# Optimization experiments

Measured on AMD Instinct MI355X. Metric: run time of the kernel, lower is better.

The kernel has to match this reference:

```python
import jax, jax.numpy as jnp
import numpy as np

K = 9
KS = (K - 1) // 2  # k_self
C_LIGHT = 299792458.0 / 1e6 / 600.0  # speed of light in detector units (as in HLayer)
BN_EPS = 1e-3  # keras BatchNormalization default epsilon


def _win2(f):
    # (B, N) -> (B, N, K): out[b, n, k] = f[b, n + k - KS], zero-padded at boundaries
    B, N = f.shape
    fp = jnp.pad(f, ((0, 0), (KS, KS)))
    return jnp.stack([fp[:, k:k + N] for k in range(K)], axis=2)


def _win3(f):
    # (B, N, F) -> (B, N, K, F): same shift-window along N
    B, N, F = f.shape
    fp = jnp.pad(f, ((0, 0), (KS, KS), (0, 0)))
    return jnp.stack([fp[:, k:k + N, :] for k in range(K)], axis=2)


def _valid_mask(N):
    # (N, K): True where neighbor index n + k - KS is in range
    idx = jnp.arange(N)[:, None] + jnp.arange(K)[None, :] - KS
    return (idx >= 0) & (idx < N)


def _hlayer(x):
    # x: (B, N, 6) with cols (t, c, a, px, py, pz) -> (B, N, K, 12)
    t, c, a = x[..., 0], x[..., 1], x[..., 2]
    px, py, pz = x[..., 3], x[..., 4], x[..., 5]
    N = x.shape[1]
    valid = _valid_mask(N)[None, :, :]  # (1, N, K)

    def d(f):  # shifted minus self, zeroed at boundaries (matches TF pad of the diff)
        return jnp.where(valid, _win2(f) - f[:, :, None], 0.0)

    dt, dx, dy, dz = d(t), d(px), d(py), d(pz)
    eu2 = dx * dx + dy * dy + dz * dz
    euclidean = jnp.sqrt(eu2)
    lorentz = (C_LIGHT * dt) ** 2 - eu2
    feats = [_win2(t), _win2(px), _win2(py), _win2(pz), _win2(c), _win2(a),
             dt, dx, dy, dz, euclidean, lorentz]
    return jnp.stack(feats, axis=3)  # (B, N, K, 12)


def _conv_bn(x, W, b, gamma, beta, mean, var):
    # kernel-size-1 Conv1D with relu activation, then inference-mode BatchNorm
    y = jax.nn.relu(jnp.matmul(x, W) + b)
    return gamma * (y - mean) * jax.lax.rsqrt(var + BN_EPS) + beta


def _make_params(key, dims):
    params = {}
    for i, (fi, fo) in enumerate(zip(dims[:-1], dims[1:])):
        key, k1 = jax.random.split(key)
        s = np.sqrt(2.0 / fi)
        params[f'W{i}'] = jax.random.normal(k1, (fi, fo), jnp.float32) * s
        params[f'b{i}'] = jnp.zeros((fo,), jnp.float32)
        key, k2, k3, k4 = jax.random.split(key, 4)
        params[f'g{i}'] = 1.0 + 0.1 * jax.random.normal(k2, (fo,), jnp.float32)
        params[f'be{i}'] = 0.1 * jax.random.normal(k3, (fo,), jnp.float32)
        params[f'mu{i}'] = 0.1 * jax.random.normal(k4, (fo,), jnp.float32)
        params[f'var{i}'] = 0.5 + jax.random.uniform(key, (fo,), jnp.float32)
    return params


def setup_inputs() -> dict:
    key = jax.random.key(0)
    kx, km, kf = jax.random.split(key, 3)
    B, N = 8, 4096
    x = jax.random.normal(kx, (B, N, 6), jnp.float32)
    dims_m = [12, 128, 256]   # MLayer/CRLayer stack on H features
    dims_f = [6, 128, 256]    # FRLayer stack on raw inputs
    pm = _make_params(km, dims_m)
    pf = _make_params(kf, dims_f)
    inp = {'x': x}
    for i in range(2):
        for n in ['W', 'b', 'g', 'be', 'mu', 'var']:
            inp[f'm_{n}{i}'] = pm[f'{n}{i}']
            inp[f'f_{n}{i}'] = pf[f'{n}{i}']
    return inp


def reference(x,
              m_W0, m_b0, m_g0, m_be0, m_mu0, m_var0,
              m_W1, m_b1, m_g1, m_be1, m_mu1, m_var1,
              f_W0, f_b0, f_g0, f_be0, f_mu0, f_var0,
              f_W1, f_b1, f_g1, f_be1, f_mu1, f_var1):
    # H-layer: (B, N, 6) -> (B, N, K, 12) geometric neighbor features
    h = _hlayer(x)
    # M branch (CRLayer, 1x1 convs over feature dim): -> m_nkf (B, N, K, 256)
    m = _conv_bn(h, m_W0, m_b0, m_g0, m_be0, m_mu0, m_var0)
    m = _conv_bn(m, m_W1, m_b1, m_g1, m_be1, m_mu1, m_var1)
    # FR branch on raw inputs: -> fr_nf (B, N, 256)
    fr = _conv_bn(x, f_W0, f_b0, f_g0, f_be0, f_mu0, f_var0)
    fr = _conv_bn(fr, f_W1, f_b1, f_g1, f_be1, f_mu1, f_var1)
    # A-layer: gate shifted fr by m and max-aggregate over K neighbors
    fr_sh = _win3(fr)                      # (B, N, K, 256), zero-padded shifts
    T = m * fr_sh                          # (B, N, K, 256)
    return jnp.max(T, axis=2)              # (B, N, 256)
```

## Files before the change

kernel.cpp:

```cpp
#include <hip/hip_runtime.h>
#include <hip/hip_bf16.h>

#define N_PTS 4096
#define C_LIGHT 0.49965409666666664f
#define BN_EPS 1e-3f

typedef __attribute__((ext_vector_type(8))) short short8;
typedef __attribute__((ext_vector_type(4))) float f32x4;

static __device__ __forceinline__ unsigned short f2bf(float f) {
    unsigned u = __float_as_uint(f);
    u += 0x7FFFu + ((u >> 16) & 1u);
    return (unsigned short)(u >> 16);
}
static __device__ __forceinline__ float bf2f(unsigned short h) {
    return __uint_as_float(((unsigned)h) << 16);
}
static __device__ __forceinline__ unsigned pk2(float a, float b) {
    __hip_bfloat162 h = __float22bfloat162_rn(make_float2(a, b));
    union { __hip_bfloat162 v; unsigned u; } cv;
    cv.v = h;
    return cv.u;
}

__global__ __launch_bounds__(256) void fold_kernel(
    const float* __restrict__ mW1, const float* __restrict__ mb1,
    const float* __restrict__ mg0, const float* __restrict__ mbe0,
    const float* __restrict__ mmu0, const float* __restrict__ mvar0,
    const float* __restrict__ mg1, const float* __restrict__ mbe1,
    const float* __restrict__ mmu1, const float* __restrict__ mvar1,
    const float* __restrict__ fW1p, const float* __restrict__ fb1,
    const float* __restrict__ fg0, const float* __restrict__ fbe0,
    const float* __restrict__ fmu0, const float* __restrict__ fvar0,
    const float* __restrict__ fg1, const float* __restrict__ fbe1,
    const float* __restrict__ fmu1, const float* __restrict__ fvar1,
    float* __restrict__ mBf, float* __restrict__ mS1, float* __restrict__ mT1,
    unsigned short* __restrict__ mWhi, unsigned short* __restrict__ mWlo,
    float* __restrict__ fBf, float* __restrict__ fS1, float* __restrict__ fT1,
    unsigned short* __restrict__ fWhi, unsigned short* __restrict__ fWlo)
{
    int br = blockIdx.x;
    const float* W1  = br ? fW1p : mW1;
    const float* b1  = br ? fb1  : mb1;
    const float* g0  = br ? fg0  : mg0;
    const float* be0 = br ? fbe0 : mbe0;
    const float* mu0 = br ? fmu0 : mmu0;
    const float* var0= br ? fvar0: mvar0;
    const float* g1  = br ? fg1  : mg1;
    const float* be1 = br ? fbe1 : mbe1;
    const float* mu1 = br ? fmu1 : mmu1;
    const float* var1= br ? fvar1: mvar1;
    float* Bf = br ? fBf : mBf;
    float* S1 = br ? fS1 : mS1;
    float* T1 = br ? fT1 : mT1;
    unsigned short* Whi = br ? fWhi : mWhi;
    unsigned short* Wlo = br ? fWlo : mWlo;

    __shared__ float s0s[128], t0s[128];
    int t = threadIdx.x;
    if (t < 128) {
        float s = g0[t] / sqrtf(var0[t] + BN_EPS);
        s0s[t] = s;
        t0s[t] = be0[t] - mu0[t] * s;
    }
    __syncthreads();

    {
        float s1 = g1[t] / sqrtf(var1[t] + BN_EPS);
        S1[t] = s1;
        T1[t] = be1[t] - mu1[t] * s1;
        float acc = b1[t];
        for (int i = 0; i < 128; ++i) acc = fmaf(t0s[i], W1[i * 256 + t], acc);
        Bf[t] = acc;
    }

    for (int e = t; e < 32768; e += 256) {
        int j = e & 7, l = (e >> 3) & 63, ks = (e >> 9) & 3, ct = e >> 11;
        int i = ks * 32 + (l >> 4) * 8 + j;
        int c = ct * 16 + (l & 15);
        float w = s0s[i] * W1[i * 256 + c];
        unsigned short hi = f2bf(w);
        unsigned short lo = f2bf(w - bf2f(hi));
        Whi[e] = hi;
        Wlo[e] = lo;
    }
}

__global__ __launch_bounds__(256, 2) void fr_kernel(
    const float* __restrict__ x,
    const float* __restrict__ W0,
    const float* __restrict__ b0,
    const short8* __restrict__ WfHi, const short8* __restrict__ WfLo,
    const float* __restrict__ Bf, const float* __restrict__ S1,
    const float* __restrict__ T1,
    float* __restrict__ frT)
{
    __shared__ float xs[64][6];
    __shared__ __attribute__((aligned(16))) float w0s[6][136];
    __shared__ __attribute__((aligned(16))) float b0s[128];
    __shared__ __attribute__((aligned(16))) unsigned short hAhi[4 * 64 * 8];
    __shared__ __attribute__((aligned(16))) unsigned short hAlo[4 * 64 * 8];

    int t = threadIdx.x;
    long row0 = (long)blockIdx.x * 64;

    for (int i = t; i < 384; i += 256) xs[i / 6][i % 6] = x[row0 * 6 + i];
    for (int i = t; i < 768; i += 256) w0s[i >> 7][i & 127] = W0[i];
    if (t < 128) b0s[t] = b0[t];

    int lane = t & 63, wv = t >> 6;
    int laneN = lane & 15, laneH = lane >> 4;
    int cg = t & 7;

    float bfv[4], s1v[4], t1v[4];
    int colc[4];
#pragma unroll
    for (int c = 0; c < 4; ++c) {
        colc[c] = (wv * 4 + c) * 16 + laneN;
        bfv[c] = Bf[colc[c]];
        s1v[c] = S1[colc[c]];
        t1v[c] = T1[colc[c]];
    }
    f32x4 acc[4][4];
#pragma unroll
    for (int mt = 0; mt < 4; ++mt)
#pragma unroll
        for (int c = 0; c < 4; ++c) {
            f32x4 z = {bfv[c], bfv[c], bfv[c], bfv[c]};
            acc[mt][c] = z;
        }
    __syncthreads();

    for (int ks = 0; ks < 4; ++ks) {
        int k0 = ks * 32 + cg * 4;
        float4 wreg[6];
#pragma unroll
        for (int i = 0; i < 6; ++i) wreg[i] = *(const float4*)&w0s[i][k0];
        float4 bq = *(const float4*)&b0s[k0];

        for (int idx = t; idx < 512; idx += 256) {
            int row = idx >> 3;
            float a0 = bq.x, a1 = bq.y, a2 = bq.z, a3 = bq.w;
#pragma unroll
            for (int i = 0; i < 6; ++i) {
                float hv = xs[row][i];
                a0 = fmaf(hv, wreg[i].x, a0);
                a1 = fmaf(hv, wreg[i].y, a1);
                a2 = fmaf(hv, wreg[i].z, a2);
                a3 = fmaf(hv, wreg[i].w, a3);
            }
            a0 = fmaxf(a0, 0.f); a1 = fmaxf(a1, 0.f);
            a2 = fmaxf(a2, 0.f); a3 = fmaxf(a3, 0.f);
            unsigned hi01 = pk2(a0, a1), hi23 = pk2(a2, a3);
            float q0 = __uint_as_float(hi01 << 16);
            float q1 = __uint_as_float(hi01 & 0xffff0000u);
            float q2 = __uint_as_float(hi23 << 16);
            float q3 = __uint_as_float(hi23 & 0xffff0000u);
            unsigned lo01 = pk2(a0 - q0, a1 - q1), lo23 = pk2(a2 - q2, a3 - q3);
            int mt = row >> 4, nl = row & 15;
            int base = (mt * 64 + (cg >> 1) * 16 + nl) * 8 + (cg & 1) * 4;
            *(uint2*)&hAhi[base] = make_uint2(hi01, hi23);
            *(uint2*)&hAlo[base] = make_uint2(lo01, lo23);
        }
        __syncthreads();

        short8 Bhi[4], Blo[4];
#pragma unroll
        for (int c = 0; c < 4; ++c) {
            int fo = ((wv * 4 + c) * 4 + ks) * 64 + lane;
            Bhi[c] = WfHi[fo];
            Blo[c] = WfLo[fo];
        }
#pragma unroll
        for (int mt = 0; mt < 4; ++mt) {
            short8 Ahi = *(const short8*)&hAhi[(mt * 64 + lane) * 8];
            short8 Alo = *(const short8*)&hAlo[(mt * 64 + lane) * 8];
#pragma unroll
            for (int c = 0; c < 4; ++c) {
                f32x4 a = acc[mt][c];
                a = __builtin_amdgcn_mfma_f32_16x16x32_bf16(Alo, Bhi[c], a, 0, 0, 0);
                a = __builtin_amdgcn_mfma_f32_16x16x32_bf16(Ahi, Blo[c], a, 0, 0, 0);
                a = __builtin_amdgcn_mfma_f32_16x16x32_bf16(Ahi, Bhi[c], a, 0, 0, 0);
                acc[mt][c] = a;
            }
        }
        __syncthreads();
    }

#pragma unroll
    for (int c = 0; c < 4; ++c)
#pragma unroll
        for (int mt = 0; mt < 4; ++mt) {
            float4 o;
            o.x = fmaf(fmaxf(acc[mt][c][0], 0.f), s1v[c], t1v[c]);
            o.y = fmaf(fmaxf(acc[mt][c][1], 0.f), s1v[c], t1v[c]);
            o.z = fmaf(fmaxf(acc[mt][c][2], 0.f), s1v[c], t1v[c]);
            o.w = fmaf(fmaxf(acc[mt][c][3], 0.f), s1v[c], t1v[c]);
            *(float4*)&frT[(long)colc[c] * 32768 + row0 + mt * 16 + laneH * 4] = o;
        }
}

#define SM_XS   0
#define SM_B0   576
#define SM_W0   1088
#define SM_HF   7616
#define SM_AHI  14528
#define SM_ALO  23744
#define SM_FRT  0
#define SM_OUT  33792
#define SM_TOT  50432

__global__ __launch_bounds__(256, 2) void fused_kernel(
    const float* __restrict__ x,
    const float* __restrict__ W0,
    const float* __restrict__ b0,
    const short8* __restrict__ WfHi, const short8* __restrict__ WfLo,
    const float* __restrict__ Bf, const float* __restrict__ S1,
    const float* __restrict__ T1,
    const float* __restrict__ frT,
    float* __restrict__ out)
{
    __shared__ __attribute__((aligned(16))) char smem[SM_TOT];
    float* xs  = (float*)(smem + SM_XS);
    float* b0s = (float*)(smem + SM_B0);
    float* w0s = (float*)(smem + SM_W0);
    float* hfp = (float*)(smem + SM_HF);
    unsigned short* hAhi = (unsigned short*)(smem + SM_AHI);
    unsigned short* hAlo = (unsigned short*)(smem + SM_ALO);
    float* frL = (float*)(smem + SM_FRT);
    float* oL  = (float*)(smem + SM_OUT);

    int t = threadIdx.x;
    int bn = blockIdx.x;
    int b  = bn >> 8;
    int n0 = (bn & 255) << 4;
    const float* xb = x + (long)b * N_PTS * 6;

    if (t < 144) {
        int rr = t / 6, cc = t % 6;
        int n = n0 - 4 + rr;
        xs[rr * 6 + cc] = (n >= 0 && n < N_PTS) ? xb[n * 6 + cc] : 0.f;
    }
    for (int i = t; i < 12 * 128; i += 256) w0s[(i >> 7) * 136 + (i & 127)] = W0[i];
    if (t < 128) b0s[t] = b0[t];
    __syncthreads();

    if (t < 144) {
        int kt = t >> 4, nl = t & 15;
        const float* self = &xs[(nl + 4) * 6];
        const float* nb   = &xs[(nl + kt) * 6];
        int nbn = n0 + nl + kt - 4;
        float msk = (nbn >= 0 && nbn < N_PTS) ? 1.f : 0.f;
        float dt = (nb[0] - self[0]) * msk;
        float dx = (nb[3] - self[3]) * msk;
        float dy = (nb[4] - self[4]) * msk;
        float dz = (nb[5] - self[5]) * msk;
        float eu2 = dx * dx + dy * dy + dz * dz;
        float* h = &hfp[t * 12];
        h[0]  = nb[0];
        h[1]  = nb[3];
        h[2]  = nb[4];
        h[3]  = nb[5];
        h[4]  = nb[1];
        h[5]  = nb[2];
        h[6]  = dt;
        h[7]  = dx;
        h[8]  = dy;
        h[9]  = dz;
        h[10] = sqrtf(eu2);
        float cdt = C_LIGHT * dt;
        h[11] = cdt * cdt - eu2;
    }

    int lane = t & 63, wv = t >> 6;
    int laneN = lane & 15, laneH = lane >> 4;
    int cg = t & 7;

    float bfv[4], s1v[4], t1v[4];
    int colc[4];
#pragma unroll
    for (int c = 0; c < 4; ++c) {
        colc[c] = (wv * 4 + c) * 16 + laneN;
        bfv[c] = Bf[colc[c]];
        s1v[c] = S1[colc[c]];
        t1v[c] = T1[colc[c]];
    }
    f32x4 acc[9][4];
#pragma unroll
    for (int kt = 0; kt < 9; ++kt)
#pragma unroll
        for (int c = 0; c < 4; ++c) {
            f32x4 z = {bfv[c], bfv[c], bfv[c], bfv[c]};
            acc[kt][c] = z;
        }
    __syncthreads();

    for (int ks = 0; ks < 4; ++ks) {
        int k0 = ks * 32 + cg * 4;
        float4 wreg[12];
#pragma unroll
        for (int i = 0; i < 12; ++i) wreg[i] = *(const float4*)&w0s[i * 136 + k0];
        float4 bq = *(const float4*)&b0s[k0];

        for (int idx = t; idx < 1152; idx += 256) {
            int row = idx >> 3;
            float a0 = bq.x, a1 = bq.y, a2 = bq.z, a3 = bq.w;
#pragma unroll
            for (int i = 0; i < 12; ++i) {
                float hv = hfp[row * 12 + i];
                a0 = fmaf(hv, wreg[i].x, a0);
                a1 = fmaf(hv, wreg[i].y, a1);
                a2 = fmaf(hv, wreg[i].z, a2);
                a3 = fmaf(hv, wreg[i].w, a3);
            }
            a0 = fmaxf(a0, 0.f); a1 = fmaxf(a1, 0.f);
            a2 = fmaxf(a2, 0.f); a3 = fmaxf(a3, 0.f);
            unsigned hi01 = pk2(a0, a1), hi23 = pk2(a2, a3);
            float q0 = __uint_as_float(hi01 << 16);
            float q1 = __uint_as_float(hi01 & 0xffff0000u);
            float q2 = __uint_as_float(hi23 << 16);
            float q3 = __uint_as_float(hi23 & 0xffff0000u);
            unsigned lo01 = pk2(a0 - q0, a1 - q1), lo23 = pk2(a2 - q2, a3 - q3);
            int kt = row >> 4, nl = row & 15;
            int base = (kt * 64 + (cg >> 1) * 16 + nl) * 8 + (cg & 1) * 4;
            *(uint2*)&hAhi[base] = make_uint2(hi01, hi23);
            *(uint2*)&hAlo[base] = make_uint2(lo01, lo23);
        }
        __syncthreads();

        short8 Bhi[4], Blo[4];
#pragma unroll
        for (int c = 0; c < 4; ++c) {
            int fo = ((wv * 4 + c) * 4 + ks) * 64 + lane;
            Bhi[c] = WfHi[fo];
            Blo[c] = WfLo[fo];
        }
#pragma unroll
        for (int kt = 0; kt < 9; ++kt) {
            short8 Ahi = *(const short8*)&hAhi[(kt * 64 + lane) * 8];
            short8 Alo = *(const short8*)&hAlo[(kt * 64 + lane) * 8];
#pragma unroll
            for (int c = 0; c < 4; ++c) {
                f32x4 a = acc[kt][c];
                a = __builtin_amdgcn_mfma_f32_16x16x32_bf16(Alo, Bhi[c], a, 0, 0, 0);
                a = __builtin_amdgcn_mfma_f32_16x16x32_bf16(Ahi, Blo[c], a, 0, 0, 0);
                a = __builtin_amdgcn_mfma_f32_16x16x32_bf16(Ahi, Bhi[c], a, 0, 0, 0);
                acc[kt][c] = a;
            }
        }
        __syncthreads();
    }
    for (int i = t; i < 2048; i += 256) {
        int col = i >> 3, seg = i & 7;
        int nn = n0 - 8 + seg * 4;
        float4 v = make_float4(0.f, 0.f, 0.f, 0.f);
        if (nn >= 0 && nn < N_PTS)
            v = *(const float4*)&frT[(long)col * 32768 + (b << 12) + nn];
        *(float4*)&frL[col * 33 + seg * 4] = v;
    }
    __syncthreads();

#pragma unroll
    for (int c = 0; c < 4; ++c) {
        float fv[12];
        int fb = colc[c] * 33 + laneH * 4 + 4;
#pragma unroll
        for (int j = 0; j < 12; ++j) fv[j] = frL[fb + j];
#pragma unroll
        for (int r = 0; r < 4; ++r) {
            float best;
#pragma unroll
            for (int kt = 0; kt < 9; ++kt) {
                float m = fmaf(fmaxf(acc[kt][c][r], 0.f), s1v[c], t1v[c]);
                float T = m * fv[r + kt];
                best = (kt == 0) ? T : fmaxf(best, T);
            }
            oL[(laneH * 4 + r) * 260 + colc[c]] = best;
        }
    }
    __syncthreads();

    float* outb = out + ((long)b << 20);
    for (int i = t; i < 1024; i += 256) {
        int row = i >> 6, c4 = (i & 63) << 2;
        float4 v = *(const float4*)&oL[row * 260 + c4];
        *(float4*)&outb[((long)(n0 + row) << 8) + c4] = v;
    }
}

extern "C" void kernel_launch(void* const* d_in, const int* in_sizes, int n_in,
                              void* d_out, int out_size, void* d_ws, size_t ws_size,
                              hipStream_t stream)
{
    const float* x = (const float*)d_in[0];
    const float* m_W0  = (const float*)d_in[1];
    const float* f_W0  = (const float*)d_in[2];
    const float* m_b0  = (const float*)d_in[3];
    const float* f_b0  = (const float*)d_in[4];
    const float* m_g0  = (const float*)d_in[5];
    const float* f_g0  = (const float*)d_in[6];
    const float* m_be0 = (const float*)d_in[7];
    const float* f_be0 = (const float*)d_in[8];
    const float* m_mu0 = (const float*)d_in[9];
    const float* f_mu0 = (const float*)d_in[10];
    const float* m_var0= (const float*)d_in[11];
    const float* f_var0= (const float*)d_in[12];
    const float* m_W1  = (const float*)d_in[13];
    const float* f_W1  = (const float*)d_in[14];
    const float* m_b1  = (const float*)d_in[15];
    const float* f_b1  = (const float*)d_in[16];
    const float* m_g1  = (const float*)d_in[17];
    const float* f_g1  = (const float*)d_in[18];
    const float* m_be1 = (const float*)d_in[19];
    const float* f_be1 = (const float*)d_in[20];
    const float* m_mu1 = (const float*)d_in[21];
    const float* f_mu1 = (const float*)d_in[22];
    const float* m_var1= (const float*)d_in[23];
    const float* f_var1= (const float*)d_in[24];

    char* wsb = (char*)d_ws;
    float* frT = (float*)wsb;
    float* mBf = (float*)(wsb + 33554432);
    float* mS1 = mBf + 256;
    float* mT1 = mS1 + 256;
    float* fBf = mT1 + 256;
    float* fS1 = fBf + 256;
    float* fT1 = fS1 + 256;
    unsigned short* mWhi = (unsigned short*)(fT1 + 256);
    unsigned short* mWlo = mWhi + 32768;
    unsigned short* fWhi = mWlo + 32768;
    unsigned short* fWlo = fWhi + 32768;

    fold_kernel<<<2, 256, 0, stream>>>(
        m_W1, m_b1, m_g0, m_be0, m_mu0, m_var0, m_g1, m_be1, m_mu1, m_var1,
        f_W1, f_b1, f_g0, f_be0, f_mu0, f_var0, f_g1, f_be1, f_mu1, f_var1,
        mBf, mS1, mT1, mWhi, mWlo,
        fBf, fS1, fT1, fWhi, fWlo);

    fr_kernel<<<8 * N_PTS / 64, 256, 0, stream>>>(
        x, f_W0, f_b0, (const short8*)fWhi, (const short8*)fWlo,
        fBf, fS1, fT1, frT);

    fused_kernel<<<8 * N_PTS / 16, 256, 0, stream>>>(
        x, m_W0, m_b0, (const short8*)mWhi, (const short8*)mWlo,
        mBf, mS1, mT1, frT, (float*)d_out);
}
```

Baseline: 239.6 us.

## Fuse FR branch into main kernel with halo recompute and parallelize weight folding

```diff
diff --git a/kernel.cpp b/kernel.cpp
--- a/kernel.cpp
+++ b/kernel.cpp
@@ -23,7 +23,7 @@
     return cv.u;
 }
 
-__global__ __launch_bounds__(256) void fold_kernel(
+__global__ __launch_bounds__(256) void fold_all(
     const float* __restrict__ mW1, const float* __restrict__ mb1,
     const float* __restrict__ mg0, const float* __restrict__ mbe0,
     const float* __restrict__ mmu0, const float* __restrict__ mvar0,
@@ -35,200 +35,106 @@
     const float* __restrict__ fg1, const float* __restrict__ fbe1,
     const float* __restrict__ fmu1, const float* __restrict__ fvar1,
     float* __restrict__ mBf, float* __restrict__ mS1, float* __restrict__ mT1,
+    float* __restrict__ fBf, float* __restrict__ fS1, float* __restrict__ fT1,
     unsigned short* __restrict__ mWhi, unsigned short* __restrict__ mWlo,
-    float* __restrict__ fBf, float* __restrict__ fS1, float* __restrict__ fT1,
     unsigned short* __restrict__ fWhi, unsigned short* __restrict__ fWlo)
 {
-    int br = blockIdx.x;
-    const float* W1  = br ? fW1p : mW1;
-    const float* b1  = br ? fb1  : mb1;
-    const float* g0  = br ? fg0  : mg0;
-    const float* be0 = br ? fbe0 : mbe0;
-    const float* mu0 = br ? fmu0 : mmu0;
-    const float* var0= br ? fvar0: mvar0;
-    const float* g1  = br ? fg1  : mg1;
-    const float* be1 = br ? fbe1 : mbe1;
-    const float* mu1 = br ? fmu1 : mmu1;
-    const float* var1= br ? fvar1: mvar1;
-    float* Bf = br ? fBf : mBf;
-    float* S1 = br ? fS1 : mS1;
-    float* T1 = br ? fT1 : mT1;
-    unsigned short* Whi = br ? fWhi : mWhi;
-    unsigned short* Wlo = br ? fWlo : mWlo;
-
-    __shared__ float s0s[128], t0s[128];
+    int bid = blockIdx.x;
     int t = threadIdx.x;
-    if (t < 128) {
-        float s = g0[t] / sqrtf(var0[t] + BN_EPS);
-        s0s[t] = s;
-        t0s[t] = be0[t] - mu0[t] * s;
-    }
-    __syncthreads();
-
-    {
+
+    if (bid < 2) {
+        int br = bid;
+        const float* W1  = br ? fW1p : mW1;
+        const float* b1  = br ? fb1  : mb1;
+        const float* g0  = br ? fg0  : mg0;
+        const float* be0 = br ? fbe0 : mbe0;
+        const float* mu0 = br ? fmu0 : mmu0;
+        const float* var0= br ? fvar0: mvar0;
+        const float* g1  = br ? fg1  : mg1;
+        const float* be1 = br ? fbe1 : mbe1;
+        const float* mu1 = br ? fmu1 : mmu1;
+        const float* var1= br ? fvar1: mvar1;
+        float* Bf = br ? fBf : mBf;
+        float* S1 = br ? fS1 : mS1;
+        float* T1 = br ? fT1 : mT1;
+
+        __shared__ float t0s[128];
+        if (t < 128) {
+            float s = g0[t] / sqrtf(var0[t] + BN_EPS);
+            t0s[t] = be0[t] - mu0[t] * s;
+        }
+        __syncthreads();
+
         float s1 = g1[t] / sqrtf(var1[t] + BN_EPS);
         S1[t] = s1;
         T1[t] = be1[t] - mu1[t] * s1;
         float acc = b1[t];
         for (int i = 0; i < 128; ++i) acc = fmaf(t0s[i], W1[i * 256 + t], acc);
         Bf[t] = acc;
-    }
-
-    for (int e = t; e < 32768; e += 256) {
-        int j = e & 7, l = (e >> 3) & 63, ks = (e >> 9) & 3, ct = e >> 11;
-        int i = ks * 32 + (l >> 4) * 8 + j;
+    } else {
+        int wbid = bid - 2;
+        int br = wbid >> 4, blk = wbid & 15;
+        const float* W1  = br ? fW1p : mW1;
+        const float* g0  = br ? fg0  : mg0;
+        const float* var0= br ? fvar0: mvar0;
+        unsigned short* Whi = br ? fWhi : mWhi;
+        unsigned short* Wlo = br ? fWlo : mWlo;
+
+        __shared__ float s0s[128];
+        if (t < 128) s0s[t] = g0[t] / sqrtf(var0[t] + BN_EPS);
+        __syncthreads();
+
+        int e0 = blk * 2048 + t * 8;
+        int l = (e0 >> 3) & 63, ks = (e0 >> 9) & 3, ct = e0 >> 11;
         int c = ct * 16 + (l & 15);
-        float w = s0s[i] * W1[i * 256 + c];
-        unsigned short hi = f2bf(w);
-        unsigned short lo = f2bf(w - bf2f(hi));
-        Whi[e] = hi;
-        Wlo[e] = lo;
-    }
-}
-
-__global__ __launch_bounds__(256, 2) void fr_kernel(
-    const float* __restrict__ x,
-    const float* __restrict__ W0,
-    const float* __restrict__ b0,
-    const short8* __restrict__ WfHi, const short8* __restrict__ WfLo,
-    const float* __restrict__ Bf, const float* __restrict__ S1,
-    const float* __restrict__ T1,
-    float* __restrict__ frT)
-{
-    __shared__ float xs[64][6];
-    __shared__ __attribute__((aligned(16))) float w0s[6][136];
-    __shared__ __attribute__((aligned(16))) float b0s[128];
-    __shared__ __attribute__((aligned(16))) unsigned short hAhi[4 * 64 * 8];
-    __shared__ __attribute__((aligned(16))) unsigned short hAlo[4 * 64 * 8];
-
-    int t = threadIdx.x;
-    long row0 = (long)blockIdx.x * 64;
-
-    for (int i = t; i < 384; i += 256) xs[i / 6][i % 6] = x[row0 * 6 + i];
-    for (int i = t; i < 768; i += 256) w0s[i >> 7][i & 127] = W0[i];
-    if (t < 128) b0s[t] = b0[t];
-
-    int lane = t & 63, wv = t >> 6;
-    int laneN = lane & 15, laneH = lane >> 4;
-    int cg = t & 7;
-
-    float bfv[4], s1v[4], t1v[4];
-    int colc[4];
-#pragma unroll
-    for (int c = 0; c < 4; ++c) {
-        colc[c] = (wv * 4 + c) * 16 + laneN;
-        bfv[c] = Bf[colc[c]];
-        s1v[c] = S1[colc[c]];
-        t1v[c] = T1[colc[c]];
-    }
-    f32x4 acc[4][4];
-#pragma unroll
-    for (int mt = 0; mt < 4; ++mt)
-#pragma unroll
-        for (int c = 0; c < 4; ++c) {
-            f32x4 z = {bfv[c], bfv[c], bfv[c], bfv[c]};
-            acc[mt][c] = z;
-        }
-    __syncthreads();
-
-    for (int ks = 0; ks < 4; ++ks) {
-        int k0 = ks * 32 + cg * 4;
-        float4 wreg[6];
-#pragma unroll
-        for (int i = 0; i < 6; ++i) wreg[i] = *(const float4*)&w0s[i][k0];
-        float4 bq = *(const float4*)&b0s[k0];
-
-        for (int idx = t; idx < 512; idx += 256) {
-            int row = idx >> 3;
-            float a0 = bq.x, a1 = bq.y, a2 = bq.z, a3 = bq.w;
-#pragma unroll
-            for (int i = 0; i < 6; ++i) {
-                float hv = xs[row][i];
-                a0 = fmaf(hv, wreg[i].x, a0);
-                a1 = fmaf(hv, wreg[i].y, a1);
-                a2 = fmaf(hv, wreg[i].z, a2);
-                a3 = fmaf(hv, wreg[i].w, a3);
-            }
-            a0 = fmaxf(a0, 0.f); a1 = fmaxf(a1, 0.f);
-            a2 = fmaxf(a2, 0.f); a3 = fmaxf(a3, 0.f);
-            unsigned hi01 = pk2(a0, a1), hi23 = pk2(a2, a3);
-            float q0 = __uint_as_float(hi01 << 16);
-            float q1 = __uint_as_float(hi01 & 0xffff0000u);
-            float q2 = __uint_as_float(hi23 << 16);
-            float q3 = __uint_as_float(hi23 & 0xffff0000u);
-            unsigned lo01 = pk2(a0 - q0, a1 - q1), lo23 = pk2(a2 - q2, a3 - q3);
-            int mt = row >> 4, nl = row & 15;
-            int base = (mt * 64 + (cg >> 1) * 16 + nl) * 8 + (cg & 1) * 4;
-            *(uint2*)&hAhi[base] = make_uint2(hi01, hi23);
-            *(uint2*)&hAlo[base] = make_uint2(lo01, lo23);
-        }
-        __syncthreads();
-
-        short8 Bhi[4], Blo[4];
-#pragma unroll
-        for (int c = 0; c < 4; ++c) {
-            int fo = ((wv * 4 + c) * 4 + ks) * 64 + lane;
-            Bhi[c] = WfHi[fo];
-            Blo[c] = WfLo[fo];
-        }
-#pragma unroll
-        for (int mt = 0; mt < 4; ++mt) {
-            short8 Ahi = *(const short8*)&hAhi[(mt * 64 + lane) * 8];
-            short8 Alo = *(const short8*)&hAlo[(mt * 64 + lane) * 8];
-#pragma unroll
-            for (int c = 0; c < 4; ++c) {
-                f32x4 a = acc[mt][c];
-                a = __builtin_amdgcn_mfma_f32_16x16x32_bf16(Alo, Bhi[c], a, 0, 0, 0);
-                a = __builtin_amdgcn_mfma_f32_16x16x32_bf16(Ahi, Blo[c], a, 0, 0, 0);
-                a = __builtin_amdgcn_mfma_f32_16x16x32_bf16(Ahi, Bhi[c], a, 0, 0, 0);
-                acc[mt][c] = a;
-            }
-        }
-        __syncthreads();
-    }
-
-#pragma unroll
-    for (int c = 0; c < 4; ++c)
-#pragma unroll
-        for (int mt = 0; mt < 4; ++mt) {
-            float4 o;
-            o.x = fmaf(fmaxf(acc[mt][c][0], 0.f), s1v[c], t1v[c]);
-            o.y = fmaf(fmaxf(acc[mt][c][1], 0.f), s1v[c], t1v[c]);
-            o.z = fmaf(fmaxf(acc[mt][c][2], 0.f), s1v[c], t1v[c]);
-            o.w = fmaf(fmaxf(acc[mt][c][3], 0.f), s1v[c], t1v[c]);
-            *(float4*)&frT[(long)colc[c] * 32768 + row0 + mt * 16 + laneH * 4] = o;
-        }
-}
-
-#define SM_XS   0
-#define SM_B0   576
-#define SM_W0   1088
-#define SM_HF   7616
-#define SM_AHI  14528
-#define SM_ALO  23744
-#define SM_FRT  0
-#define SM_OUT  33792
-#define SM_TOT  50432
+        int ib = ks * 32 + (l >> 4) * 8;
+        unsigned short hi[8], lo[8];
+#pragma unroll
+        for (int j = 0; j < 8; ++j) {
+            float w = s0s[ib + j] * W1[(ib + j) * 256 + c];
+            hi[j] = f2bf(w);
+            lo[j] = f2bf(w - bf2f(hi[j]));
+        }
+        *(uint4*)&Whi[e0] = *(uint4*)hi;
+        *(uint4*)&Wlo[e0] = *(uint4*)lo;
+    }
+}
+
+#define SM_XS    0
+#define SM_B0F   768
+#define SM_W0F   1280
+#define SM_B0M   4544
+#define SM_W0M   5056
+#define SM_HF    11584
+#define SM_FRFRG 18496
+#define SM_MFRG  22592
+#define SM_OUT   22592
+#define SM_FRL   41024
+#define SM_TOT   74304
 
 __global__ __launch_bounds__(256, 2) void fused_kernel(
     const float* __restrict__ x,
-    const float* __restrict__ W0,
-    const float* __restrict__ b0,
-    const short8* __restrict__ WfHi, const short8* __restrict__ WfLo,
-    const float* __restrict__ Bf, const float* __restrict__ S1,
-    const float* __restrict__ T1,
-    const float* __restrict__ frT,
+    const float* __restrict__ mW0,
+    const float* __restrict__ mb0,
+    const float* __restrict__ fW0,
+    const float* __restrict__ fb0,
+    const short8* __restrict__ mWfHi, const short8* __restrict__ mWfLo,
+    const short8* __restrict__ fWfHi, const short8* __restrict__ fWfLo,
+    const float* __restrict__ mBf, const float* __restrict__ mS1,
+    const float* __restrict__ mT1,
+    const float* __restrict__ fBf, const float* __restrict__ fS1,
+    const float* __restrict__ fT1,
     float* __restrict__ out)
 {
     __shared__ __attribute__((aligned(16))) char smem[SM_TOT];
-    float* xs  = (float*)(smem + SM_XS);
-    float* b0s = (float*)(smem + SM_B0);
-    float* w0s = (float*)(smem + SM_W0);
-    float* hfp = (float*)(smem + SM_HF);
-    unsigned short* hAhi = (unsigned short*)(smem + SM_AHI);
-    unsigned short* hAlo = (unsigned short*)(smem + SM_ALO);
-    float* frL = (float*)(smem + SM_FRT);
-    float* oL  = (float*)(smem + SM_OUT);
+    float* xs   = (float*)(smem + SM_XS);
+    float* b0f  = (float*)(smem + SM_B0F);
+    float* w0f  = (float*)(smem + SM_W0F);
+    float* b0m  = (float*)(smem + SM_B0M);
+    float* w0m  = (float*)(smem + SM_W0M);
+    float* hfp  = (float*)(smem + SM_HF);
+    float* frL  = (float*)(smem + SM_FRL);
+    float* oL   = (float*)(smem + SM_OUT);
 
     int t = threadIdx.x;
     int bn = blockIdx.x;
@@ -236,19 +142,20 @@
     int n0 = (bn & 255) << 4;
     const float* xb = x + (long)b * N_PTS * 6;
 
-    if (t < 144) {
+    if (t < 192) {
         int rr = t / 6, cc = t % 6;
-        int n = n0 - 4 + rr;
+        int n = n0 - 8 + rr;
         xs[rr * 6 + cc] = (n >= 0 && n < N_PTS) ? xb[n * 6 + cc] : 0.f;
     }
-    for (int i = t; i < 12 * 128; i += 256) w0s[(i >> 7) * 136 + (i & 127)] = W0[i];
-    if (t < 128) b0s[t] = b0[t];
+    for (int i = t; i < 768; i += 256)  w0f[(i >> 7) * 136 + (i & 127)] = fW0[i];
+    for (int i = t; i < 1536; i += 256) w0m[(i >> 7) * 136 + (i & 127)] = mW0[i];
+    if (t < 128) { b0f[t] = fb0[t]; b0m[t] = mb0[t]; }
     __syncthreads();
 
     if (t < 144) {
         int kt = t >> 4, nl = t & 15;
-        const float* self = &xs[(nl + 4) * 6];
-        const float* nb   = &xs[(nl + kt) * 6];
+        const float* self = &xs[(nl + 8) * 6];
+        const float* nb   = &xs[(nl + kt + 4) * 6];
         int nbn = n0 + nl + kt - 4;
         float msk = (nbn >= 0 && nbn < N_PTS) ? 1.f : 0.f;
         float dt = (nb[0] - self[0]) * msk;
@@ -275,70 +182,154 @@
     int lane = t & 63, wv = t >> 6;
     int laneN = lane & 15, laneH = lane >> 4;
     int cg = t & 7;
-
-    float bfv[4], s1v[4], t1v[4];
+    int rowh = t >> 3;
+
     int colc[4];
 #pragma unroll
-    for (int c = 0; c < 4; ++c) {
-        colc[c] = (wv * 4 + c) * 16 + laneN;
-        bfv[c] = Bf[colc[c]];
-        s1v[c] = S1[colc[c]];
-        t1v[c] = T1[colc[c]];
-    }
+    for (int c = 0; c < 4; ++c) colc[c] = (wv * 4 + c) * 16 + laneN;
+
+    {
+        unsigned short* Fhi = (unsigned short*)(smem + SM_FRFRG);
+        unsigned short* Flo = Fhi + 2048;
+
+        f32x4 accF[2][4];
+#pragma unroll
+        for (int mt = 0; mt < 2; ++mt)
+#pragma unroll
+            for (int c = 0; c < 4; ++c) {
+                float bv = fBf[colc[c]];
+                f32x4 z = {bv, bv, bv, bv};
+                accF[mt][c] = z;
+            }
+
+        for (int ks = 0; ks < 4; ++ks) {
+            if (ks) __syncthreads();
+            {
+                int k0 = ks * 32 + cg * 4;
+                float a0 = b0f[k0], a1 = b0f[k0+1], a2 = b0f[k0+2], a3 = b0f[k0+3];
+#pragma unroll
+                for (int i = 0; i < 6; ++i) {
+                    float hv = xs[rowh * 6 + i];
+                    a0 = fmaf(hv, w0f[i * 136 + k0],     a0);
+                    a1 = fmaf(hv, w0f[i * 136 + k0 + 1], a1);
+                    a2 = fmaf(hv, w0f[i * 136 + k0 + 2], a2);
+                    a3 = fmaf(hv, w0f[i * 136 + k0 + 3], a3);
+                }
+                a0 = fmaxf(a0, 0.f); a1 = fmaxf(a1, 0.f);
+                a2 = fmaxf(a2, 0.f); a3 = fmaxf(a3, 0.f);
+                unsigned hi01 = pk2(a0, a1), hi23 = pk2(a2, a3);
+                float q0 = __uint_as_float(hi01 << 16);
+                float q1 = __uint_as_float(hi01 & 0xffff0000u);
+                float q2 = __uint_as_float(hi23 << 16);
+                float q3 = __uint_as_float(hi23 & 0xffff0000u);
+                unsigned lo01 = pk2(a0 - q0, a1 - q1), lo23 = pk2(a2 - q2, a3 - q3);
+                int mt = rowh >> 4, nl2 = rowh & 15;
+                int base = (mt * 64 + (cg >> 1) * 16 + nl2) * 8 + (cg & 1) * 4;
+                *(uint2*)&Fhi[base] = make_uint2(hi01, hi23);
+                *(uint2*)&Flo[base] = make_uint2(lo01, lo23);
+            }
+            __syncthreads();
+            short8 Bhi[4], Blo[4];
+#pragma unroll
+            for (int c = 0; c < 4; ++c) {
+                int fo = ((wv * 4 + c) * 4 + ks) * 64 + lane;
+                Bhi[c] = fWfHi[fo];
+                Blo[c] = fWfLo[fo];
+            }
+#pragma unroll
+            for (int mt = 0; mt < 2; ++mt) {
+                short8 Ahi = *(const short8*)&Fhi[(mt * 64 + lane) * 8];
+                short8 Alo = *(const short8*)&Flo[(mt * 64 + lane) * 8];
+#pragma unroll
+                for (int c = 0; c < 4; ++c) {
+                    f32x4 a = accF[mt][c];
+                    a = __builtin_amdgcn_mfma_f32_16x16x32_bf16(Alo, Bhi[c], a, 0, 0, 0);
+                    a = __builtin_amdgcn_mfma_f32_16x16x32_bf16(Ahi, Blo[c], a, 0, 0, 0);
+                    a = __builtin_amdgcn_mfma_f32_16x16x32_bf16(Ahi, Bhi[c], a, 0, 0, 0);
+                    accF[mt][c] = a;
+                }
+            }
+        }
+
+#pragma unroll
+        for (int c = 0; c < 4; ++c) {
+            float s1 = fS1[colc[c]], t1 = fT1[colc[c]];
+#pragma unroll
+            for (int mt = 0; mt < 2; ++mt)
+#pragma unroll
+                for (int r = 0; r < 4; ++r) {
+                    int rl = mt * 16 + laneH * 4 + r;
+                    int nn = n0 - 8 + rl;
+                    float y = fmaf(fmaxf(accF[mt][c][r], 0.f), s1, t1);
+                    frL[rl * 260 + colc[c]] =
+                        (nn >= 0 && nn < N_PTS) ? y : 0.f;
+                }
+        }
+    }
+    __syncthreads();
+
+    float s1v[4], t1v[4];
+#pragma unroll
+    for (int c = 0; c < 4; ++c) { s1v[c] = mS1[colc[c]]; t1v[c] = mT1[colc[c]]; }
+
     f32x4 acc[9][4];
 #pragma unroll
     for (int kt = 0; kt < 9; ++kt)
 #pragma unroll
         for (int c = 0; c < 4; ++c) {
-            f32x4 z = {bfv[c], bfv[c], bfv[c], bfv[c]};
+            float bv = mBf[colc[c]];
+            f32x4 z = {bv, bv, bv, bv};
             acc[kt][c] = z;
         }
-    __syncthreads();
+
+    unsigned short* Hhi = (unsigned short*)(smem + SM_MFRG);
+    unsigned short* Hlo = Hhi + 4608;
 
     for (int ks = 0; ks < 4; ++ks) {
-        int k0 = ks * 32 + cg * 4;
-        float4 wreg[12];
-#pragma unroll
-        for (int i = 0; i < 12; ++i) wreg[i] = *(const float4*)&w0s[i * 136 + k0];
-        float4 bq = *(const float4*)&b0s[k0];
-
-        for (int idx = t; idx < 1152; idx += 256) {
-            int row = idx >> 3;
-            float a0 = bq.x, a1 = bq.y, a2 = bq.z, a3 = bq.w;
-#pragma unroll
-            for (int i = 0; i < 12; ++i) {
-                float hv = hfp[row * 12 + i];
-                a0 = fmaf(hv, wreg[i].x, a0);
-                a1 = fmaf(hv, wreg[i].y, a1);
-                a2 = fmaf(hv, wreg[i].z, a2);
-                a3 = fmaf(hv, wreg[i].w, a3);
-            }
-            a0 = fmaxf(a0, 0.f); a1 = fmaxf(a1, 0.f);
-            a2 = fmaxf(a2, 0.f); a3 = fmaxf(a3, 0.f);
-            unsigned hi01 = pk2(a0, a1), hi23 = pk2(a2, a3);
-            float q0 = __uint_as_float(hi01 << 16);
-            float q1 = __uint_as_float(hi01 & 0xffff0000u);
-            float q2 = __uint_as_float(hi23 << 16);
-            float q3 = __uint_as_float(hi23 & 0xffff0000u);
-            unsigned lo01 = pk2(a0 - q0, a1 - q1), lo23 = pk2(a2 - q2, a3 - q3);
-            int kt = row >> 4, nl = row & 15;
-            int base = (kt * 64 + (cg >> 1) * 16 + nl) * 8 + (cg & 1) * 4;
-            *(uint2*)&hAhi[base] = make_uint2(hi01, hi23);
-            *(uint2*)&hAlo[base] = make_uint2(lo01, lo23);
+        if (ks) __syncthreads();
+        {
+            int k0 = ks * 32 + cg * 4;
+            float4 wreg[12];
+#pragma unroll
+            for (int i = 0; i < 12; ++i) wreg[i] = *(const float4*)&w0m[i * 136 + k0];
+            float4 bq = *(const float4*)&b0m[k0];
+            for (int idx = t; idx < 1152; idx += 256) {
+                int row = idx >> 3;
+                float a0 = bq.x, a1 = bq.y, a2 = bq.z, a3 = bq.w;
+#pragma unroll
+                for (int i = 0; i < 12; ++i) {
+                    float hv = hfp[row * 12 + i];
+                    a0 = fmaf(hv, wreg[i].x, a0);
+                    a1 = fmaf(hv, wreg[i].y, a1);
+                    a2 = fmaf(hv, wreg[i].z, a2);
+                    a3 = fmaf(hv, wreg[i].w, a3);
+                }
+                a0 = fmaxf(a0, 0.f); a1 = fmaxf(a1, 0.f);
+                a2 = fmaxf(a2, 0.f); a3 = fmaxf(a3, 0.f);
+                unsigned hi01 = pk2(a0, a1), hi23 = pk2(a2, a3);
+                float q0 = __uint_as_float(hi01 << 16);
+                float q1 = __uint_as_float(hi01 & 0xffff0000u);
+                float q2 = __uint_as_float(hi23 << 16);
+                float q3 = __uint_as_float(hi23 & 0xffff0000u);
+                unsigned lo01 = pk2(a0 - q0, a1 - q1), lo23 = pk2(a2 - q2, a3 - q3);
+                int kt = row >> 4, nl = row & 15;
+                int base = (kt * 64 + (cg >> 1) * 16 + nl) * 8 + (cg & 1) * 4;
+                *(uint2*)&Hhi[base] = make_uint2(hi01, hi23);
+                *(uint2*)&Hlo[base] = make_uint2(lo01, lo23);
+            }
         }
         __syncthreads();
-
         short8 Bhi[4], Blo[4];
 #pragma unroll
         for (int c = 0; c < 4; ++c) {
             int fo = ((wv * 4 + c) * 4 + ks) * 64 + lane;
-            Bhi[c] = WfHi[fo];
-            Blo[c] = WfLo[fo];
+            Bhi[c] = mWfHi[fo];
+            Blo[c] = mWfLo[fo];
         }
 #pragma unroll
         for (int kt = 0; kt < 9; ++kt) {
-            short8 Ahi = *(const short8*)&hAhi[(kt * 64 + lane) * 8];
-            short8 Alo = *(const short8*)&hAlo[(kt * 64 + lane) * 8];
+            short8 Ahi = *(const short8*)&Hhi[(kt * 64 + lane) * 8];
+            short8 Alo = *(const short8*)&Hlo[(kt * 64 + lane) * 8];
 #pragma unroll
             for (int c = 0; c < 4; ++c) {
                 f32x4 a = acc[kt][c];
@@ -348,24 +339,15 @@
                 acc[kt][c] = a;
             }
         }
-        __syncthreads();
-    }
-    for (int i = t; i < 2048; i += 256) {
-        int col = i >> 3, seg = i & 7;
-        int nn = n0 - 8 + seg * 4;
-        float4 v = make_float4(0.f, 0.f, 0.f, 0.f);
-        if (nn >= 0 && nn < N_PTS)
-            v = *(const float4*)&frT[(long)col * 32768 + (b << 12) + nn];
-        *(float4*)&frL[col * 33 + seg * 4] = v;
     }
     __syncthreads();
 
 #pragma unroll
     for (int c = 0; c < 4; ++c) {
         float fv[12];
-        int fb = colc[c] * 33 + laneH * 4 + 4;
-#pragma unroll
-        for (int j = 0; j < 12; ++j) fv[j] = frL[fb + j];
+        int fb = (laneH * 4 + 4) * 260 + colc[c];
+#pragma unroll
+        for (int j = 0; j < 12; ++j) fv[j] = frL[fb + j * 260];
 #pragma unroll
         for (int r = 0; r < 4; ++r) {
             float best;
@@ -418,9 +400,8 @@
     const float* m_var1= (const float*)d_in[23];
     const float* f_var1= (const float*)d_in[24];
 
-    char* wsb = (char*)d_ws;
-    float* frT = (float*)wsb;
-    float* mBf = (float*)(wsb + 33554432);
+    float* ws  = (float*)d_ws;
+    float* mBf = ws;
     float* mS1 = mBf + 256;
     float* mT1 = mS1 + 256;
     float* fBf = mT1 + 256;
@@ -431,17 +412,16 @@
     unsigned short* fWhi = mWlo + 32768;
     unsigned short* fWlo = fWhi + 32768;
 
-    fold_kernel<<<2, 256, 0, stream>>>(
+    fold_all<<<34, 256, 0, stream>>>(
         m_W1, m_b1, m_g0, m_be0, m_mu0, m_var0, m_g1, m_be1, m_mu1, m_var1,
         f_W1, f_b1, f_g0, f_be0, f_mu0, f_var0, f_g1, f_be1, f_mu1, f_var1,
-        mBf, mS1, mT1, mWhi, mWlo,
-        fBf, fS1, fT1, fWhi, fWlo);
-
-    fr_kernel<<<8 * N_PTS / 64, 256, 0, stream>>>(
-        x, f_W0, f_b0, (const short8*)fWhi, (const short8*)fWlo,
-        fBf, fS1, fT1, frT);
+        mBf, mS1, mT1, fBf, fS1, fT1,
+        mWhi, mWlo, fWhi, fWlo);
 
     fused_kernel<<<8 * N_PTS / 16, 256, 0, stream>>>(
-        x, m_W0, m_b0, (const short8*)mWhi, (const short8*)mWlo,
-        mBf, mS1, mT1, frT, (float*)d_out);
-}
+        x, m_W0, m_b0, f_W0, f_b0,
+        (const short8*)mWhi, (const short8*)mWlo,
+        (const short8*)fWhi, (const short8*)fWlo,
+        mBf, mS1, mT1, fBf, fS1, fT1,
+        (float*)d_out);
+}
```

New measurement: 199.5 us. -16.7%, faster.
